# Kernel tuning notes

Hardware: AMD Instinct MI355X
Metric: run time of the kernel (lower is better)

The kernel has to match this reference:

```python
import jax, jax.numpy as jnp
import numpy as np

B, T, H, K = 64, 512, 768, 11
START_ID, END_ID = 9, 10  # tag_to_ix['<CLS>'], tag_to_ix['<SEP>']
NEG = -10000.0


def setup_inputs() -> dict:
    key = jax.random.key(0)
    k1, k2, k3, k4 = jax.random.split(key, 4)
    embeds = jax.random.normal(k1, (B, T, H), dtype=jnp.float32)
    W_fc = jax.random.normal(k2, (K, H), dtype=jnp.float32) * 0.02
    b_fc = jax.random.normal(k3, (K,), dtype=jnp.float32) * 0.02
    transitions = jax.random.normal(k4, (K, K), dtype=jnp.float32)
    # __init__ masking: no transition out of anything into START row, none into END col
    transitions = transitions.at[START_ID, :].set(NEG)
    transitions = transitions.at[:, END_ID].set(NEG)
    return {"embeds": embeds, "W_fc": W_fc, "b_fc": b_fc, "transitions": transitions}


def reference(embeds, W_fc, b_fc, transitions):
    # fc projection: feats[b,t,k] (PLM_crf path: encoder output -> Linear)
    feats = jnp.einsum('bth,kh->btk', embeds, W_fc) + b_fc  # [B,T,K]
    Bv, Tv, Kv = feats.shape

    # Viterbi: log_delta init -10000 except start tag; NOTE the original never
    # adds feats[:, 0] (loop starts at t=1), so we faithfully skip it too.
    log_delta0 = jnp.full((Bv, Kv), NEG, dtype=feats.dtype).at[:, START_ID].set(0.0)

    def step(log_delta, feat_t):
        # transitions[i, j]: score of moving from prev tag j to tag i
        scores = transitions[None, :, :] + log_delta[:, None, :]  # [B,K,K]
        psi_t = jnp.argmax(scores, axis=-1)                       # [B,K] best prev tag
        log_delta_new = jnp.max(scores, axis=-1) + feat_t         # [B,K]
        return log_delta_new, psi_t

    feats_seq = jnp.swapaxes(feats[:, 1:], 0, 1)                  # [T-1,B,K]
    log_delta, psi = jax.lax.scan(step, log_delta0, feats_seq)    # psi: [T-1,B,K]

    score = jnp.max(log_delta, axis=-1)                           # [B]
    last_tag = jnp.argmax(log_delta, axis=-1)                     # [B]

    # Backtrack: path[t] = psi[t+1][path[t+1]] for t = T-2 .. 0
    def back(next_tag, psi_t):
        tag = jnp.take_along_axis(psi_t, next_tag[:, None], axis=-1)[:, 0]
        return tag, tag

    _, path_rest = jax.lax.scan(back, last_tag, psi, reverse=True)  # [T-1,B]
    path = jnp.concatenate([jnp.swapaxes(path_rest, 0, 1), last_tag[:, None]], axis=1)  # [B,T]
    return score, path
```

## Files before the change

kernel.cpp:

```cpp
#include <hip/hip_runtime.h>

#define BB 64
#define TT 512
#define HH 768
#define KK 11
#define START_ID 9
#define NEGV -10000.0f
#define TT4 (TT + 4)

typedef float vf2 __attribute__((ext_vector_type(2)));

template <int CTRL>
__device__ __forceinline__ float dpp_add(float x) {
    int yi = __builtin_amdgcn_update_dpp(0, __float_as_int(x), CTRL, 0xF, 0xF, false);
    return x + __int_as_float(yi);
}

__device__ __forceinline__ float wave_sum_to_lane63(float x) {
    x = dpp_add<0x111>(x);
    x = dpp_add<0x112>(x);
    x = dpp_add<0x114>(x);
    x = dpp_add<0x118>(x);
    x = dpp_add<0x142>(x);
    x = dpp_add<0x143>(x);
    return x;
}

__device__ __forceinline__ float rlane(float v, int l) {
    return __int_as_float(__builtin_amdgcn_readlane(__float_as_int(v), l));
}

__global__ __launch_bounds__(256) void fc_kernel(const float* __restrict__ embeds,
                                                 const float* __restrict__ W,
                                                 const float* __restrict__ bias,
                                                 float* __restrict__ feats) {
    __shared__ __align__(16) float w_lds[KK * HH];

    const int tid = threadIdx.x;
    const int lane = tid & 63;

    {
        const float4* src = reinterpret_cast<const float4*>(W);
        float4* dst = reinterpret_cast<float4*>(w_lds);
#pragma unroll
        for (int i = 0; i < 9; ++i) {
            int idx = tid + i * 256;
            if (idx < KK * HH / 4) dst[idx] = src[idx];
        }
    }

    float bk[KK];
#pragma unroll
    for (int k = 0; k < KK; ++k) bk[k] = bias[k];

    __syncthreads();

    const int wave_id = (blockIdx.x * blockDim.x + tid) >> 6;
    const int base = wave_id * 8;
    const int lo = lane * 4;

    const float* ea = embeds + (size_t)base * HH;
    const float* eb = ea + HH;
    float4 a0 = *reinterpret_cast<const float4*>(ea + 0   + lo);
    float4 a1 = *reinterpret_cast<const float4*>(ea + 256 + lo);
    float4 a2 = *reinterpret_cast<const float4*>(ea + 512 + lo);
    float4 b0 = *reinterpret_cast<const float4*>(eb + 0   + lo);
    float4 b1 = *reinterpret_cast<const float4*>(eb + 256 + lo);
    float4 b2 = *reinterpret_cast<const float4*>(eb + 512 + lo);

#pragma unroll 1
    for (int rr = 0; rr < 8; rr += 2) {
        const int nrr = (rr + 2) & 7;
        const float* na = embeds + (size_t)(base + nrr) * HH;
        const float* nb = na + HH;
        float4 na0 = *reinterpret_cast<const float4*>(na + 0   + lo);
        float4 na1 = *reinterpret_cast<const float4*>(na + 256 + lo);
        float4 na2 = *reinterpret_cast<const float4*>(na + 512 + lo);
        float4 nb0 = *reinterpret_cast<const float4*>(nb + 0   + lo);
        float4 nb1 = *reinterpret_cast<const float4*>(nb + 256 + lo);
        float4 nb2 = *reinterpret_cast<const float4*>(nb + 512 + lo);

        vf2 va[6] = {{a0.x, a0.y}, {a0.z, a0.w}, {a1.x, a1.y},
                     {a1.z, a1.w}, {a2.x, a2.y}, {a2.z, a2.w}};
        vf2 vb[6] = {{b0.x, b0.y}, {b0.z, b0.w}, {b1.x, b1.y},
                     {b1.z, b1.w}, {b2.x, b2.y}, {b2.z, b2.w}};

        float4 w0 = *reinterpret_cast<const float4*>(w_lds + 0 + lo);
        float4 w1 = *reinterpret_cast<const float4*>(w_lds + 256 + lo);
        float4 w2 = *reinterpret_cast<const float4*>(w_lds + 512 + lo);

        float rA[KK], rB[KK];
#pragma unroll
        for (int k = 0; k < KK; ++k) {
            const int nk = (k == KK - 1) ? 0 : k + 1;
            float4 nw0 = *reinterpret_cast<const float4*>(w_lds + nk * HH + 0 + lo);
            float4 nw1 = *reinterpret_cast<const float4*>(w_lds + nk * HH + 256 + lo);
            float4 nw2 = *reinterpret_cast<const float4*>(w_lds + nk * HH + 512 + lo);

            vf2 wv[6] = {{w0.x, w0.y}, {w0.z, w0.w},
                         {w1.x, w1.y}, {w1.z, w1.w},
                         {w2.x, w2.y}, {w2.z, w2.w}};
            vf2 sA = va[0] * wv[0];
            vf2 sB = vb[0] * wv[0];
#pragma unroll
            for (int r = 1; r < 6; ++r) { sA += va[r] * wv[r]; sB += vb[r] * wv[r]; }
            rA[k] = wave_sum_to_lane63(sA.x + sA.y);
            rB[k] = wave_sum_to_lane63(sB.x + sB.y);

            w0 = nw0; w1 = nw1; w2 = nw2;
        }

        if (lane == 63) {
            float* oA = feats + (size_t)(base + rr) * KK;
#pragma unroll
            for (int k = 0; k < KK; ++k) oA[k] = rA[k] + bk[k];
#pragma unroll
            for (int k = 0; k < KK; ++k) oA[KK + k] = rB[k] + bk[k];
        }

        a0 = na0; a1 = na1; a2 = na2;
        b0 = nb0; b1 = nb1; b2 = nb2;
    }
}

__global__ __launch_bounds__(256) void viterbi_kernel(const float* __restrict__ feats,
                                                      const float* __restrict__ trans,
                                                      float* __restrict__ out) {
    __shared__ __align__(16) float featsT[KK * TT4];
    __shared__ __align__(16) float dh[(TT - 1) * 12 + 16];
    __shared__ int psi_lds[(TT - 1) * KK];
    __shared__ float tr_lds[KK * KK];
    __shared__ int comp[15 * KK];
    __shared__ int bt[16];
    __shared__ int sh_last;

    const int tid = threadIdx.x;
    const int b = blockIdx.x;

    {
        const float4* src = reinterpret_cast<const float4*>(feats + (size_t)b * TT * KK);
        for (int idx4 = tid; idx4 < TT * KK / 4; idx4 += 256) {
            float4 v = src[idx4];
            const int e = idx4 * 4;
#pragma unroll
            for (int u = 0; u < 4; ++u) {
                int t = (e + u) / KK;
                int k = (e + u) - t * KK;
                if (t > 0) featsT[k * TT4 + (t - 1)] = (&v.x)[u];
            }
        }
        if (tid < KK * KK) tr_lds[tid] = trans[tid];
    }
    __syncthreads();

    if (tid < 64) {
        const int i = tid;
        float tr[KK];
#pragma unroll
        for (int j = 0; j < KK; ++j) tr[j] = (i < KK) ? tr_lds[i * KK + j] : NEGV;

        float delta = (i == START_ID) ? 0.0f : NEGV;

        int dhoff = (i < KK) ? i : (TT - 1) * 12;
        const int dhstep = (i < KK) ? 12 : 0;

        auto vstep = [&](float fcur) {
            dh[dhoff] = delta;
            dhoff += dhstep;
            float dj[KK];
#pragma unroll
            for (int j = 0; j < KK; ++j) dj[j] = rlane(delta, j);
            float s[KK];
#pragma unroll
            for (int j = 0; j < KK; ++j) s[j] = tr[j] + dj[j];
            float t0 = fmaxf(fmaxf(s[0], s[1]), s[2]);
            float t1 = fmaxf(fmaxf(s[3], s[4]), s[5]);
            float t2 = fmaxf(fmaxf(s[6], s[7]), s[8]);
            float t3 = fmaxf(s[9], s[10]);
            float best = fmaxf(fmaxf(fmaxf(t0, t1), t2), t3);
            delta = best + fcur;
        };

        auto chunk16 = [&](const float4& f0, const float4& f1,
                           const float4& f2, const float4& f3) {
            vstep(f0.x); vstep(f0.y); vstep(f0.z); vstep(f0.w);
            vstep(f1.x); vstep(f1.y); vstep(f1.z); vstep(f1.w);
            vstep(f2.x); vstep(f2.y); vstep(f2.z); vstep(f2.w);
            vstep(f3.x); vstep(f3.y); vstep(f3.z); vstep(f3.w);
        };

        const int ci = (i < KK) ? i : 0;
        const float* frow = featsT + ci * TT4;

        float4 A0 = *reinterpret_cast<const float4*>(frow + 0);
        float4 A1 = *reinterpret_cast<const float4*>(frow + 4);
        float4 A2 = *reinterpret_cast<const float4*>(frow + 8);
        float4 A3 = *reinterpret_cast<const float4*>(frow + 12);

#pragma unroll 1
        for (int c = 0; c < 31; ++c) {
            const float* nf = frow + (c + 1) * 16;
            float4 B0 = *reinterpret_cast<const float4*>(nf + 0);
            float4 B1 = *reinterpret_cast<const float4*>(nf + 4);
            float4 B2 = *reinterpret_cast<const float4*>(nf + 8);
            float4 B3 = *reinterpret_cast<const float4*>(nf + 12);

            chunk16(A0, A1, A2, A3);

            A0 = B0; A1 = B1; A2 = B2; A3 = B3;
        }
        vstep(A0.x); vstep(A0.y); vstep(A0.z); vstep(A0.w);
        vstep(A1.x); vstep(A1.y); vstep(A1.z); vstep(A1.w);
        vstep(A2.x); vstep(A2.y); vstep(A2.z); vstep(A2.w);
        vstep(A3.x); vstep(A3.y); vstep(A3.z);

        float dfin[KK];
#pragma unroll
        for (int j = 0; j < KK; ++j) dfin[j] = rlane(delta, j);
        float best = dfin[0];
        int last = 0;
#pragma unroll
        for (int j = 1; j < KK; ++j) {
            bool c = dfin[j] > best;
            best = c ? dfin[j] : best;
            last = c ? j : last;
        }
        if (tid == 0) {
            out[b] = best;
            out[BB + (size_t)b * TT + (TT - 1)] = (float)last;
            sh_last = last;
        }
    }
    __syncthreads();

    {
        const int i = tid & 15;
        const int sg = tid >> 4;
        if (i < KK) {
            float tri[KK];
#pragma unroll
            for (int j = 0; j < KK; ++j) tri[j] = tr_lds[i * KK + j];
            for (int s = sg; s < TT - 1; s += 16) {
                const float4* dr = reinterpret_cast<const float4*>(dh + s * 12);
                float4 a = dr[0], c4 = dr[1], d4 = dr[2];
                float sc[KK] = {tri[0] + a.x,  tri[1] + a.y,  tri[2] + a.z,  tri[3] + a.w,
                                tri[4] + c4.x, tri[5] + c4.y, tri[6] + c4.z, tri[7] + c4.w,
                                tri[8] + d4.x, tri[9] + d4.y, tri[10] + d4.z};
                float bv = sc[0];
                int bj = 0;
#pragma unroll
                for (int j = 1; j < KK; ++j) {
                    bool c = sc[j] > bv;
                    bv = c ? sc[j] : bv;
                    bj = c ? j : bj;
                }
                psi_lds[s * KK + i] = bj;
            }
        }
    }
    __syncthreads();

    {
        const int c = tid >> 4;
        const int i = tid & 15;
        if (c < 15 && i < KK) {
            int cur = i;
            for (int s = c * 32 + 31; s >= c * 32; --s) cur = psi_lds[s * KK + cur];
            comp[c * KK + i] = cur;
        } else if (c == 15 && i == 0) {
            int cur = sh_last;
            float* po = out + BB + (size_t)b * TT;
            for (int s = TT - 2; s >= 480; --s) {
                cur = psi_lds[s * KK + cur];
                po[s] = (float)cur;
            }
            bt[15] = cur;
        }
    }
    __syncthreads();

    if (tid == 0) {
        for (int c = 14; c >= 1; --c) bt[c] = comp[c * KK + bt[c + 1]];
    }
    __syncthreads();

    if (tid < 15) {
        const int c = tid;
        int cur = bt[c + 1];
        float* po = out + BB + (size_t)b * TT;
        for (int s = c * 32 + 31; s >= c * 32; --s) {
            cur = psi_lds[s * KK + cur];
            po[s] = (float)cur;
        }
    }
}

extern "C" void kernel_launch(void* const* d_in, const int* in_sizes, int n_in,
                              void* d_out, int out_size, void* d_ws, size_t ws_size,
                              hipStream_t stream) {
    const float* embeds = (const float*)d_in[0];
    const float* W_fc   = (const float*)d_in[1];
    const float* b_fc   = (const float*)d_in[2];
    const float* trans  = (const float*)d_in[3];
    float* out = (float*)d_out;
    float* feats = (float*)d_ws;

    fc_kernel<<<1024, 256, 0, stream>>>(embeds, W_fc, b_fc, feats);
    viterbi_kernel<<<BB, 256, 0, stream>>>(feats, trans, out);
}
```

Baseline: 198.5 us.

## Split Viterbi into forward and backtrack kernels via global delta history

Splits the single Viterbi kernel into a forward-recursion kernel and a separate argmax/backtrack kernel. The forward kernel writes its per-step delta history to a workspace buffer in global memory, and the back kernel reloads it. This shrinks each kernel's shared memory footprint, which may help occupancy or launch. The cost is an extra launch plus a global round trip of the delta history. It also changes the padding lanes to write distinct dummy slots.

After: 201.6 us. About the same (+1.6%).

```diff
diff --git a/kernel.cpp b/kernel.cpp
--- a/kernel.cpp
+++ b/kernel.cpp
@@ -7,6 +7,8 @@
 #define START_ID 9
 #define NEGV -10000.0f
 #define TT4 (TT + 4)
+#define DH_REAL ((TT - 1) * 12)
+#define DH_STRIDE 6144
 
 typedef float vf2 __attribute__((ext_vector_type(2)));
 
@@ -123,16 +125,13 @@
     }
 }
 
-__global__ __launch_bounds__(256) void viterbi_kernel(const float* __restrict__ feats,
-                                                      const float* __restrict__ trans,
-                                                      float* __restrict__ out) {
+__global__ __launch_bounds__(256) void vit_fwd(const float* __restrict__ feats,
+                                               const float* __restrict__ trans,
+                                               float* __restrict__ dh_g,
+                                               float* __restrict__ out) {
     __shared__ __align__(16) float featsT[KK * TT4];
-    __shared__ __align__(16) float dh[(TT - 1) * 12 + 16];
-    __shared__ int psi_lds[(TT - 1) * KK];
+    __shared__ __align__(16) float dh[DH_REAL + 64];
     __shared__ float tr_lds[KK * KK];
-    __shared__ int comp[15 * KK];
-    __shared__ int bt[16];
-    __shared__ int sh_last;
 
     const int tid = threadIdx.x;
     const int b = blockIdx.x;
@@ -161,7 +160,7 @@
 
         float delta = (i == START_ID) ? 0.0f : NEGV;
 
-        int dhoff = (i < KK) ? i : (TT - 1) * 12;
+        int dhoff = (i < KK) ? i : (DH_REAL + (i - KK));
         const int dhstep = (i < KK) ? 12 : 0;
 
         auto vstep = [&](float fcur) {
@@ -228,8 +227,36 @@
         if (tid == 0) {
             out[b] = best;
             out[BB + (size_t)b * TT + (TT - 1)] = (float)last;
-            sh_last = last;
-        }
+        }
+    }
+    __syncthreads();
+
+    {
+        const float4* src = reinterpret_cast<const float4*>(dh);
+        float4* dst = reinterpret_cast<float4*>(dh_g + (size_t)b * DH_STRIDE);
+        for (int idx = tid; idx < DH_REAL / 4; idx += 256) dst[idx] = src[idx];
+    }
+}
+
+__global__ __launch_bounds__(256) void vit_back(const float* __restrict__ dh_g,
+                                                const float* __restrict__ trans,
+                                                float* __restrict__ out) {
+    __shared__ __align__(16) float dh[DH_REAL + 16];
+    __shared__ int psi_lds[(TT - 1) * KK];
+    __shared__ float tr_lds[KK * KK];
+    __shared__ int comp[15 * KK];
+    __shared__ int bt[16];
+    __shared__ int sh_last;
+
+    const int tid = threadIdx.x;
+    const int b = blockIdx.x;
+
+    {
+        const float4* src = reinterpret_cast<const float4*>(dh_g + (size_t)b * DH_STRIDE);
+        float4* dst = reinterpret_cast<float4*>(dh);
+        for (int idx = tid; idx < DH_REAL / 4; idx += 256) dst[idx] = src[idx];
+        if (tid < KK * KK) tr_lds[tid] = trans[tid];
+        if (tid == 0) sh_last = (int)out[BB + (size_t)b * TT + (TT - 1)];
     }
     __syncthreads();
 
@@ -304,7 +331,9 @@
     const float* trans  = (const float*)d_in[3];
     float* out = (float*)d_out;
     float* feats = (float*)d_ws;
+    float* dh_g  = (float*)((char*)d_ws + (size_t)BB * TT * KK * sizeof(float));
 
     fc_kernel<<<1024, 256, 0, stream>>>(embeds, W_fc, b_fc, feats);
-    viterbi_kernel<<<BB, 256, 0, stream>>>(feats, trans, out);
-}
+    vit_fwd<<<BB, 256, 0, stream>>>(feats, trans, dh_g, out);
+    vit_back<<<BB, 256, 0, stream>>>(dh_g, trans, out);
+}
```
